# Kernel tuning notes

Measured on AMD Instinct MI355X. Metric: run time of the kernel, lower is better.

## Reference

```python
import jax, jax.numpy as jnp
import numpy as np

RATE = 4  # mask_size=4 in MultiSequenceUpdateBlock3D


def convex_upsample(flow, mask, rate=RATE):
    """Upsample flow [N,2,H,W] -> [N,2,rate*H,rate*W] by convex combination.
    mask: [N, 9*rate*rate, H, W]."""
    N, _, H, W = flow.shape
    m = mask.reshape(N, 1, 9, rate, rate, H, W)
    m = jax.nn.softmax(m, axis=2)
    f = rate * flow
    fp = jnp.pad(f, ((0, 0), (0, 0), (1, 1), (1, 1)))
    # 3x3 unfold, row-major kernel order (matches F.unfold): (N,2,9,H,W)
    patches = jnp.stack([fp[:, :, i:i + H, j:j + W]
                         for i in range(3) for j in range(3)], axis=2)
    # (N,2,9,1,1,H,W) * (N,1,9,r,r,H,W) summed over 9 -> (N,2,r,r,H,W)
    up = jnp.sum(m * patches[:, :, :, None, None, :, :], axis=2)
    # permute (0,1,4,2,5,3) -> (N,2,H,r,W,r), reshape -> (N,2,rH,rW)
    up = up.transpose(0, 1, 4, 2, 5, 3)
    return up.reshape(N, 2, rate * H, rate * W)


def flow_warp(x, flow):
    """Warp x [N,C,H,W] by flow [N,2,H,W]; bilinear grid_sample, zeros
    padding, align_corners=True (pixel-space coords are used directly)."""
    N, C, H, W = x.shape
    gy, gx = jnp.meshgrid(jnp.arange(H, dtype=x.dtype),
                          jnp.arange(W, dtype=x.dtype), indexing='ij')
    sx = gx[None] + flow[:, 0]  # (N,H,W) sample x-coords
    sy = gy[None] + flow[:, 1]
    x0 = jnp.floor(sx); y0 = jnp.floor(sy)
    wx1 = sx - x0; wx0 = 1.0 - wx1
    wy1 = sy - y0; wy0 = 1.0 - wy1
    x_flat = x.reshape(N, C, H * W)

    def gather(xi, yi):
        valid = (xi >= 0) & (xi <= W - 1) & (yi >= 0) & (yi <= H - 1)
        xc = jnp.clip(xi, 0, W - 1).astype(jnp.int32)
        yc = jnp.clip(yi, 0, H - 1).astype(jnp.int32)
        idx = (yc * W + xc).reshape(N, 1, H * W)
        v = jnp.take_along_axis(x_flat, idx, axis=2).reshape(N, C, H, W)
        return v * valid.astype(x.dtype)[:, None]

    out = (gather(x0, y0) * (wx0 * wy0)[:, None]
           + gather(x0 + 1, y0) * (wx1 * wy0)[:, None]
           + gather(x0, y0 + 1) * (wx0 * wy1)[:, None]
           + gather(x0 + 1, y0 + 1) * (wx1 * wy1)[:, None])
    return out


def setup_inputs() -> dict:
    key = jax.random.key(0)
    k1, k2, k3 = jax.random.split(key, 3)
    N, C, H, W = 4, 64, 96, 192  # low-res grid; full res = 4H x 4W
    x = jax.random.normal(k1, (N, C, RATE * H, RATE * W), dtype=jnp.float32)
    flow = 3.0 * jax.random.normal(k2, (N, 2, H, W), dtype=jnp.float32)
    mask = jax.random.normal(k3, (N, 9 * RATE * RATE, H, W), dtype=jnp.float32)
    return {"x": x, "flow": flow, "mask": mask}


def reference(x, flow, mask):
    up_flow = convex_upsample(flow, mask, rate=RATE)
    return flow_warp(x, up_flow)
```

## Files before the change

### kernel.cpp

```cpp
#include <hip/hip_runtime.h>
#include <hip/hip_bf16.h>
#include <math.h>

constexpr int N  = 4;
constexpr int C  = 64;
constexpr int H  = 96;
constexpr int W  = 192;
constexpr int R  = 4;
constexpr int Hf = H * R;
constexpr int Wf = W * R;
constexpr int HW  = H * W;
constexpr int HWf = Hf * Wf;
constexpr size_t XT_BYTES = (size_t)N * HWf * C * sizeof(__hip_bfloat16);

__device__ __forceinline__ float bf2f(unsigned short u) {
    unsigned v = ((unsigned)u) << 16;
    float f;
    __builtin_memcpy(&f, &v, 4);
    return f;
}

__global__ __launch_bounds__(256)
void transpose_to_bf16(const float* __restrict__ x, __hip_bfloat16* __restrict__ xT) {
    __shared__ float tile[64][65];
    const int b = blockIdx.x;
    const int tilesPerN = HWf / 64;
    const int n = b / tilesPerN;
    const int pixbase = (b % tilesPerN) * 64;
    const int tid = threadIdx.x;

    const int px = tid & 63;
    const int c0 = tid >> 6;
    const float* xb = x + (size_t)n * C * HWf + pixbase;
#pragma unroll
    for (int i = 0; i < 16; ++i) {
        const int c = i * 4 + c0;
        tile[px][c] = xb[(size_t)c * HWf + px];
    }
    __syncthreads();

    const int wpx = tid >> 2;
    const int cc  = (tid & 3) * 16;
    alignas(16) __hip_bfloat16 h[16];
#pragma unroll
    for (int j = 0; j < 16; ++j)
        h[j] = __float2bfloat16(tile[wpx][cc + j]);

    uint4* dst = (uint4*)(xT + ((size_t)(n * HWf + pixbase + wpx)) * C + cc);
    const uint4* src = (const uint4*)h;
    dst[0] = src[0];
    dst[1] = src[1];
}

__global__ __launch_bounds__(256)
void fused_gather_bf16(const __hip_bfloat16* __restrict__ xT,
                       const float* __restrict__ flow,
                       const float* __restrict__ mask,
                       float* __restrict__ out) {
    int idx = blockIdx.x * blockDim.x + threadIdx.x;
    const int total = N * Hf * Wf;
    if (idx >= total) return;

    const int xpix = idx % Wf;
    int t = idx / Wf;
    const int ypix = t % Hf;
    const int n = t / Hf;

    const int w  = xpix >> 2, rj = xpix & 3;
    const int h  = ypix >> 2, ri = ypix & 3;

    const float* mbase = mask + ((size_t)n * 144 + (size_t)(ri * 4 + rj)) * HW
                              + (size_t)h * W + w;
    float mv[9];
    float mx = -INFINITY;
#pragma unroll
    for (int k = 0; k < 9; ++k) {
        mv[k] = mbase[(size_t)k * 16 * HW];
        mx = fmaxf(mx, mv[k]);
    }
    float s = 0.f;
#pragma unroll
    for (int k = 0; k < 9; ++k) {
        mv[k] = __expf(mv[k] - mx);
        s += mv[k];
    }
    const float inv = 1.0f / s;

    const float* f0 = flow + (size_t)n * 2 * HW;
    float fx = 0.f, fy = 0.f;
#pragma unroll
    for (int k = 0; k < 9; ++k) {
        const int di = k / 3 - 1;
        const int dj = k % 3 - 1;
        const int hh = h + di, ww = w + dj;
        float vx = 0.f, vy = 0.f;
        if (hh >= 0 && hh < H && ww >= 0 && ww < W) {
            const int o = hh * W + ww;
            vx = f0[o];
            vy = f0[HW + o];
        }
        const float wk = mv[k] * inv;
        fx += wk * vx;
        fy += wk * vy;
    }
    fx *= (float)R;
    fy *= (float)R;

    const float sx = (float)xpix + fx;
    const float sy = (float)ypix + fy;
    const float x0f = floorf(sx), y0f = floorf(sy);
    const int x0 = (int)x0f, y0 = (int)y0f;
    const int x1 = x0 + 1,  y1 = y0 + 1;
    const float wx1 = sx - x0f, wx0 = 1.f - wx1;
    const float wy1 = sy - y0f, wy0 = 1.f - wy1;

    const bool vx0 = (x0 >= 0) & (x0 < Wf);
    const bool vx1 = (x1 >= 0) & (x1 < Wf);
    const bool vy0 = (y0 >= 0) & (y0 < Hf);
    const bool vy1 = (y1 >= 0) & (y1 < Hf);

    const int x0c = min(max(x0, 0), Wf - 1), x1c = min(max(x1, 0), Wf - 1);
    const int y0c = min(max(y0, 0), Hf - 1), y1c = min(max(y1, 0), Hf - 1);

    const float w00 = wx0 * wy0 * (float)(vx0 & vy0);
    const float w10 = wx1 * wy0 * (float)(vx1 & vy0);
    const float w01 = wx0 * wy1 * (float)(vx0 & vy1);
    const float w11 = wx1 * wy1 * (float)(vx1 & vy1);

    const __hip_bfloat16* xb = xT + (size_t)n * HWf * C;
    const uint4* p00 = (const uint4*)(xb + (size_t)(y0c * Wf + x0c) * C);
    const uint4* p10 = (const uint4*)(xb + (size_t)(y0c * Wf + x1c) * C);
    const uint4* p01 = (const uint4*)(xb + (size_t)(y1c * Wf + x0c) * C);
    const uint4* p11 = (const uint4*)(xb + (size_t)(y1c * Wf + x1c) * C);

    float* ob = out + (size_t)n * C * HWf + (size_t)ypix * Wf + xpix;

#pragma unroll
    for (int k = 0; k < 8; ++k) {
        const uint4 a = p00[k];
        const uint4 b = p10[k];
        const uint4 c = p01[k];
        const uint4 d = p11[k];
        const unsigned short* ua = (const unsigned short*)&a;
        const unsigned short* ub = (const unsigned short*)&b;
        const unsigned short* uc = (const unsigned short*)&c;
        const unsigned short* ud = (const unsigned short*)&d;
#pragma unroll
        for (int j = 0; j < 8; ++j) {
            const float v = w00 * bf2f(ua[j]) + w10 * bf2f(ub[j])
                          + w01 * bf2f(uc[j]) + w11 * bf2f(ud[j]);
            __builtin_nontemporal_store(v, ob + (size_t)(8 * k + j) * HWf);
        }
    }
}

__global__ __launch_bounds__(256)
void fused_upsample_warp(const float* __restrict__ x,
                         const float* __restrict__ flow,
                         const float* __restrict__ mask,
                         float* __restrict__ out) {
    int idx = blockIdx.x * blockDim.x + threadIdx.x;
    const int total = N * Hf * Wf;
    if (idx >= total) return;

    const int xpix = idx % Wf;
    int t = idx / Wf;
    const int ypix = t % Hf;
    const int n = t / Hf;

    const int w  = xpix >> 2, rj = xpix & 3;
    const int h  = ypix >> 2, ri = ypix & 3;

    const float* mbase = mask + ((size_t)n * 144 + (size_t)(ri * 4 + rj)) * HW
                              + (size_t)h * W + w;
    float mv[9];
    float mx = -INFINITY;
#pragma unroll
    for (int k = 0; k < 9; ++k) {
        mv[k] = mbase[(size_t)k * 16 * HW];
        mx = fmaxf(mx, mv[k]);
    }
    float s = 0.f;
#pragma unroll
    for (int k = 0; k < 9; ++k) {
        mv[k] = __expf(mv[k] - mx);
        s += mv[k];
    }
    const float inv = 1.0f / s;

    const float* f0 = flow + (size_t)n * 2 * HW;
    float fx = 0.f, fy = 0.f;
#pragma unroll
    for (int k = 0; k < 9; ++k) {
        const int di = k / 3 - 1;
        const int dj = k % 3 - 1;
        const int hh = h + di, ww = w + dj;
        float vx = 0.f, vy = 0.f;
        if (hh >= 0 && hh < H && ww >= 0 && ww < W) {
            const int o = hh * W + ww;
            vx = f0[o];
            vy = f0[HW + o];
        }
        const float wk = mv[k] * inv;
        fx += wk * vx;
        fy += wk * vy;
    }
    fx *= (float)R;
    fy *= (float)R;

    const float sx = (float)xpix + fx;
    const float sy = (float)ypix + fy;
    const float x0f = floorf(sx), y0f = floorf(sy);
    const int x0 = (int)x0f, y0 = (int)y0f;
    const int x1 = x0 + 1,  y1 = y0 + 1;
    const float wx1 = sx - x0f, wx0 = 1.f - wx1;
    const float wy1 = sy - y0f, wy0 = 1.f - wy1;

    const bool vx0 = (x0 >= 0) & (x0 < Wf);
    const bool vx1 = (x1 >= 0) & (x1 < Wf);
    const bool vy0 = (y0 >= 0) & (y0 < Hf);
    const bool vy1 = (y1 >= 0) & (y1 < Hf);

    const int x0c = min(max(x0, 0), Wf - 1), x1c = min(max(x1, 0), Wf - 1);
    const int y0c = min(max(y0, 0), Hf - 1), y1c = min(max(y1, 0), Hf - 1);

    const float w00 = wx0 * wy0 * (float)(vx0 & vy0);
    const float w10 = wx1 * wy0 * (float)(vx1 & vy0);
    const float w01 = wx0 * wy1 * (float)(vx0 & vy1);
    const float w11 = wx1 * wy1 * (float)(vx1 & vy1);

    const size_t HWfs = (size_t)HWf;
    const float* xb = x + (size_t)n * C * HWfs;
    const size_t i00 = (size_t)y0c * Wf + x0c;
    const size_t i10 = (size_t)y0c * Wf + x1c;
    const size_t i01 = (size_t)y1c * Wf + x0c;
    const size_t i11 = (size_t)y1c * Wf + x1c;

    float* ob = out + (size_t)n * C * HWfs + (size_t)ypix * Wf + xpix;

#pragma unroll 4
    for (int c = 0; c < C; ++c) {
        const float* xc = xb + (size_t)c * HWfs;
        const float v = w00 * xc[i00] + w10 * xc[i10]
                      + w01 * xc[i01] + w11 * xc[i11];
        __builtin_nontemporal_store(v, ob + (size_t)c * HWfs);
    }
}

extern "C" void kernel_launch(void* const* d_in, const int* in_sizes, int n_in,
                              void* d_out, int out_size, void* d_ws, size_t ws_size,
                              hipStream_t stream) {
    const float* x    = (const float*)d_in[0];
    const float* flow = (const float*)d_in[1];
    const float* mask = (const float*)d_in[2];
    float* out = (float*)d_out;

    const int total = N * Hf * Wf;
    const int block = 256;
    const int grid2 = (total + block - 1) / block;

    if (ws_size >= XT_BYTES) {
        __hip_bfloat16* xT = (__hip_bfloat16*)d_ws;
        const int grid1 = N * (HWf / 64);
        transpose_to_bf16<<<grid1, block, 0, stream>>>(x, xT);
        fused_gather_bf16<<<grid2, block, 0, stream>>>(xT, flow, mask, out);
    } else {
        fused_upsample_warp<<<grid2, block, 0, stream>>>(x, flow, mask, out);
    }
}
```

Before: 764.1 us.

## Switch staging to fp16, vectorize transpose loads, tile gather blocks into 4x64 bands

The staged channels-last copy now uses fp16 instead of bf16, which gives more mantissa precision at the same footprint. The transpose kernel reads with float4 vector loads. The gather kernel maps each block to a 4-row by 64-column tile so that all threads in a block share one low-res row. Block IDs are interleaved across 8 groups, likely to spread work over XCDs and improve L2 locality for the gathers. Mask reads become nontemporal. fp16 risks overflow for large inputs, though the test inputs are normal-distributed.

```diff
diff --git a/kernel.cpp b/kernel.cpp
--- a/kernel.cpp
+++ b/kernel.cpp
@@ -1,5 +1,5 @@
 #include <hip/hip_runtime.h>
-#include <hip/hip_bf16.h>
+#include <hip/hip_fp16.h>
 #include <math.h>
 
 constexpr int N  = 4;
@@ -11,17 +11,15 @@
 constexpr int Wf = W * R;
 constexpr int HW  = H * W;
 constexpr int HWf = Hf * Wf;
-constexpr size_t XT_BYTES = (size_t)N * HWf * C * sizeof(__hip_bfloat16);
-
-__device__ __forceinline__ float bf2f(unsigned short u) {
-    unsigned v = ((unsigned)u) << 16;
-    float f;
-    __builtin_memcpy(&f, &v, 4);
-    return f;
-}
+constexpr size_t XT_BYTES = (size_t)N * HWf * C * sizeof(__half);
+
+constexpr int BANDS   = Hf / 4;
+constexpr int TCOLS   = Wf / 64;
+constexpr int BLK_IMG = BANDS * TCOLS;
+constexpr int NBLK    = N * BLK_IMG;
 
 __global__ __launch_bounds__(256)
-void transpose_to_bf16(const float* __restrict__ x, __hip_bfloat16* __restrict__ xT) {
+void transpose_to_f16(const float* __restrict__ x, __half* __restrict__ xT) {
     __shared__ float tile[64][65];
     const int b = blockIdx.x;
     const int tilesPerN = HWf / 64;
@@ -29,45 +27,53 @@
     const int pixbase = (b % tilesPerN) * 64;
     const int tid = threadIdx.x;
 
-    const int px = tid & 63;
-    const int c0 = tid >> 6;
     const float* xb = x + (size_t)n * C * HWf + pixbase;
-#pragma unroll
-    for (int i = 0; i < 16; ++i) {
-        const int c = i * 4 + c0;
-        tile[px][c] = xb[(size_t)c * HWf + px];
+    const int cg  = tid >> 4;
+    const int px4 = (tid & 15) * 4;
+#pragma unroll
+    for (int i = 0; i < 4; ++i) {
+        const int c = i * 16 + cg;
+        const float4 v = *(const float4*)(xb + (size_t)c * HWf + px4);
+        tile[px4 + 0][c] = v.x;
+        tile[px4 + 1][c] = v.y;
+        tile[px4 + 2][c] = v.z;
+        tile[px4 + 3][c] = v.w;
     }
     __syncthreads();
 
     const int wpx = tid >> 2;
-    const int cc  = (tid & 3) * 16;
-    alignas(16) __hip_bfloat16 h[16];
+    const int c0  = (tid & 3) * 16;
+    alignas(16) __half h[16];
 #pragma unroll
     for (int j = 0; j < 16; ++j)
-        h[j] = __float2bfloat16(tile[wpx][cc + j]);
-
-    uint4* dst = (uint4*)(xT + ((size_t)(n * HWf + pixbase + wpx)) * C + cc);
+        h[j] = __float2half(tile[wpx][c0 + j]);
+
+    uint4* dst = (uint4*)(xT + ((size_t)(n * HWf + pixbase + wpx)) * C + c0);
     const uint4* src = (const uint4*)h;
     dst[0] = src[0];
     dst[1] = src[1];
 }
 
 __global__ __launch_bounds__(256)
-void fused_gather_bf16(const __hip_bfloat16* __restrict__ xT,
-                       const float* __restrict__ flow,
-                       const float* __restrict__ mask,
-                       float* __restrict__ out) {
-    int idx = blockIdx.x * blockDim.x + threadIdx.x;
-    const int total = N * Hf * Wf;
-    if (idx >= total) return;
-
-    const int xpix = idx % Wf;
-    int t = idx / Wf;
-    const int ypix = t % Hf;
-    const int n = t / Hf;
+void fused_gather_f16(const __half* __restrict__ xT,
+                      const float* __restrict__ flow,
+                      const float* __restrict__ mask,
+                      float* __restrict__ out) {
+    const int bid = blockIdx.x;
+    const int l = (bid & 7) * (NBLK / 8) + (bid >> 3);
+    const int n = l / BLK_IMG;
+    const int rem = l - n * BLK_IMG;
+    const int band = rem / TCOLS;
+    const int tcol = rem - band * TCOLS;
+
+    const int ty = threadIdx.x >> 6;
+    const int tx = threadIdx.x & 63;
+    const int ypix = band * 4 + ty;
+    const int xpix = tcol * 64 + tx;
 
     const int w  = xpix >> 2, rj = xpix & 3;
-    const int h  = ypix >> 2, ri = ypix & 3;
+    const int h  = band;
+    const int ri = ty;
 
     const float* mbase = mask + ((size_t)n * 144 + (size_t)(ri * 4 + rj)) * HW
                               + (size_t)h * W + w;
@@ -75,7 +81,7 @@
     float mx = -INFINITY;
 #pragma unroll
     for (int k = 0; k < 9; ++k) {
-        mv[k] = mbase[(size_t)k * 16 * HW];
+        mv[k] = __builtin_nontemporal_load(mbase + (size_t)k * 16 * HW);
         mx = fmaxf(mx, mv[k]);
     }
     float s = 0.f;
@@ -127,7 +133,7 @@
     const float w01 = wx0 * wy1 * (float)(vx0 & vy1);
     const float w11 = wx1 * wy1 * (float)(vx1 & vy1);
 
-    const __hip_bfloat16* xb = xT + (size_t)n * HWf * C;
+    const __half* xb = xT + (size_t)n * HWf * C;
     const uint4* p00 = (const uint4*)(xb + (size_t)(y0c * Wf + x0c) * C);
     const uint4* p10 = (const uint4*)(xb + (size_t)(y0c * Wf + x1c) * C);
     const uint4* p01 = (const uint4*)(xb + (size_t)(y1c * Wf + x0c) * C);
@@ -141,14 +147,14 @@
         const uint4 b = p10[k];
         const uint4 c = p01[k];
         const uint4 d = p11[k];
-        const unsigned short* ua = (const unsigned short*)&a;
-        const unsigned short* ub = (const unsigned short*)&b;
-        const unsigned short* uc = (const unsigned short*)&c;
-        const unsigned short* ud = (const unsigned short*)&d;
+        const __half* ha = (const __half*)&a;
+        const __half* hb = (const __half*)&b;
+        const __half* hc = (const __half*)&c;
+        const __half* hd = (const __half*)&d;
 #pragma unroll
         for (int j = 0; j < 8; ++j) {
-            const float v = w00 * bf2f(ua[j]) + w10 * bf2f(ub[j])
-                          + w01 * bf2f(uc[j]) + w11 * bf2f(ud[j]);
+            const float v = w00 * __half2float(ha[j]) + w10 * __half2float(hb[j])
+                          + w01 * __half2float(hc[j]) + w11 * __half2float(hd[j]);
             __builtin_nontemporal_store(v, ob + (size_t)(8 * k + j) * HWf);
         }
     }
@@ -255,16 +261,16 @@
     const float* mask = (const float*)d_in[2];
     float* out = (float*)d_out;
 
-    const int total = N * Hf * Wf;
     const int block = 256;
-    const int grid2 = (total + block - 1) / block;
 
     if (ws_size >= XT_BYTES) {
-        __hip_bfloat16* xT = (__hip_bfloat16*)d_ws;
+        __half* xT = (__half*)d_ws;
         const int grid1 = N * (HWf / 64);
-        transpose_to_bf16<<<grid1, block, 0, stream>>>(x, xT);
-        fused_gather_bf16<<<grid2, block, 0, stream>>>(xT, flow, mask, out);
+        transpose_to_f16<<<grid1, block, 0, stream>>>(x, xT);
+        fused_gather_f16<<<NBLK, block, 0, stream>>>(xT, flow, mask, out);
     } else {
+        const int total = N * Hf * Wf;
+        const int grid2 = (total + block - 1) / block;
         fused_upsample_warp<<<grid2, block, 0, stream>>>(x, flow, mask, out);
     }
 }
```

Measured after the change: 705.5 us. -7.7%, faster.
